# Performance work log

Hardware: AMD Instinct MI355X
Metric: run time of the kernel (lower is better)

Reference implementation:

```python
import jax, jax.numpy as jnp
import numpy as np

LEN_HIS = 20   # q_len_his: sliding-window history length
DIM_C = 4      # dim_c
H = 64         # GRU hidden = final_mlp_hidden_width
D = 36         # global_graph_width(32) + goal(2) + action(2)
N = 32768      # total timesteps across many episodes


def setup_inputs() -> dict:
    key = jax.random.key(0)
    ks = jax.random.split(key, 8)
    emb = jax.random.normal(ks[0], (N, D), jnp.float32)
    dones = (jax.random.uniform(ks[1], (N, 1)) < 0.02).astype(jnp.int32)
    s = lambda k, shape, fan: jax.random.normal(k, shape, jnp.float32) / np.sqrt(fan).astype(np.float32)
    return {
        "embeddings": emb,
        "W_ih": s(ks[2], (3 * H, D), D),
        "W_hh": s(ks[3], (3 * H, H), H),
        "b_ih": jnp.zeros((3 * H,), jnp.float32),
        "b_hh": jnp.zeros((3 * H,), jnp.float32),
        "W1": s(ks[4], (H, H), H),
        "b1": jnp.zeros((H,), jnp.float32),
        "W2": s(ks[5], (DIM_C, H), H),
        "b2": jnp.zeros((DIM_C,), jnp.float32),
        "dones": dones,
    }


def _his_calculate_c(embeddings, W_ih, W_hh, b_ih, b_hh, W1, b1, W2, b2, dones):
    """Batched/padded version of the ragged sliding-window GRU+MLP loop.

    For each timestep t, the torch code runs the GRU over
    embeddings[max(episode_start, t-L+1) : t+1] from a zero hidden state,
    then applies FinalPredMLP to the final hidden state.
    """
    n = embeddings.shape[0]
    done = dones[:, 0] != 0
    idx = jnp.arange(n)
    # episode_start[t] = (index of most recent done strictly before t) + 1, else 0
    prev_done = jnp.concatenate([jnp.zeros((1,), bool), done[:-1]])
    ep_start = jax.lax.cummax(jnp.where(prev_done, idx, 0))
    win_start = jnp.maximum(ep_start, idx - LEN_HIS + 1)            # [N]

    # padded windows: position l holds embeddings[t - (L-1) + l]
    gidx = idx[:, None] - (LEN_HIS - 1) + jnp.arange(LEN_HIS)[None, :]  # [N, L]
    valid = gidx >= win_start[:, None]                                   # [N, L]
    X = embeddings[jnp.clip(gidx, 0, n - 1)] * valid[..., None]          # [N, L, D]

    def cell(h, inp):
        x, v = inp                      # x: [N, D], v: [N]
        gi = x @ W_ih.T + b_ih          # [N, 3H]
        gh = h @ W_hh.T + b_hh          # [N, 3H]
        ir, iz, inn = jnp.split(gi, 3, axis=-1)
        hr, hz, hnn = jnp.split(gh, 3, axis=-1)
        r = jax.nn.sigmoid(ir + hr)
        z = jax.nn.sigmoid(iz + hz)
        ncand = jnp.tanh(inn + r * hnn)
        h_new = (1.0 - z) * ncand + z * h
        return jnp.where(v[:, None], h_new, h), None

    h0 = jnp.zeros((n, H), embeddings.dtype)
    hT, _ = jax.lax.scan(cell, h0, (jnp.swapaxes(X, 0, 1), valid.T))  # [N, H]

    # FinalPredMLP: Linear(H,H) -> ReLU -> Linear(H, dim_c)
    hid = jax.nn.relu(hT @ W1.T + b1)
    return hid @ W2.T + b2              # [N, dim_c]


def reference(embeddings, W_ih, W_hh, b_ih, b_hh, W1, b1, W2, b2, dones):
    return _his_calculate_c(embeddings, W_ih, W_hh, b_ih, b_hh, W1, b1, W2, b2, dones)
```

## Files before the change

### kernel.cpp

```cpp
#include <hip/hip_runtime.h>

#define NT 32768
#define DI 36
#define HH 64
#define G3 192
#define LH 20
#define SGS 196

#define NLOG2E -1.4426950408889634f
#define TLOG2E 2.8853900817779268f

#define UNION_OFF  27440
#define SFIRST_OFF 41264
#define SMEM_BYTES 41328

typedef __attribute__((ext_vector_type(8))) short bf16x8;
typedef __attribute__((ext_vector_type(4))) float f32x4;
typedef __attribute__((ext_vector_type(4))) int int4v;
union frag_cast { int4v i4; bf16x8 h8; };

__device__ __forceinline__ unsigned f2u(float f) { union { float f; unsigned u; } x; x.f = f; return x.u; }
__device__ __forceinline__ float u2f(unsigned u) { union { float f; unsigned u; } x; x.u = u; return x.f; }
__device__ __forceinline__ unsigned short f2bf_rne(float f) {
    union { float f; unsigned u; } x; x.f = f;
    unsigned r = x.u + 0x7FFFu + ((x.u >> 16) & 1u);
    return (unsigned short)(r >> 16);
}

__global__ __launch_bounds__(64) void prep_kernel(
    const float* __restrict__ W_ih, const float* __restrict__ W_hh,
    int4v* __restrict__ wfrag)
{
    const int b = (int)blockIdx.x;
    const int set = b / 24, fb = b % 24;
    const int mt = fb >> 1, kt = fb & 1;
    const int l = (int)threadIdx.x;
    const int m = mt * 16 + (l & 15);
    const int g = mt >> 2;
    const float sc = (g < 2) ? NLOG2E : TLOG2E;
    const int k0 = kt * 32 + (l >> 4) * 8;
    unsigned short e[8];
#pragma unroll
    for (int jj = 0; jj < 8; ++jj) {
        const int k = k0 + jj;
        if (set == 2) {
            e[jj] = f2bf_rne(W_hh[(size_t)m * HH + k] * sc);
        } else {
            const float v = (k < DI) ? W_ih[(size_t)m * DI + k] * sc : 0.f;
            const unsigned u = f2u(v);
            if (set == 0) e[jj] = (unsigned short)(u >> 16);
            else          e[jj] = (unsigned short)(f2u(v - u2f(u & 0xFFFF0000u)) >> 16);
        }
    }
    int4v p;
    p.x = e[0] | ((unsigned)e[1] << 16); p.y = e[2] | ((unsigned)e[3] << 16);
    p.z = e[4] | ((unsigned)e[5] << 16); p.w = e[6] | ((unsigned)e[7] << 16);
    wfrag[b * 64 + l] = p;
}

__global__ __launch_bounds__(256, 3) void gru_kernel(
    const float* __restrict__ emb, const int4v* __restrict__ wfrag,
    const float* __restrict__ b_ih, const float* __restrict__ b_hh,
    const float* __restrict__ W1, const float* __restrict__ b1,
    const float* __restrict__ W2, const float* __restrict__ b2,
    const int* __restrict__ dones, float* __restrict__ out)
{
    __shared__ __align__(16) char SMEM[SMEM_BYTES];
    float* const Sg = (float*)SMEM;
    unsigned short* const EmbH = (unsigned short*)(SMEM + UNION_OFF);
    unsigned short* const EmbL = EmbH + 48 * 72;
    unsigned short* const HbB  = (unsigned short*)(SMEM + UNION_OFF);
    int* const sfirst = (int*)(SMEM + SFIRST_OFF);

    const int tid = threadIdx.x;
    const int lane = tid & 63;
    const int W = tid >> 6;
    const int li = lane & 15;
    const int q = lane >> 4;
    const int blk = ((int)blockIdx.x & 7) * 256 + ((int)blockIdx.x >> 3);
    const int T0 = blk * 16;

    {
        int4v* z = (int4v*)EmbH;
        for (int i = tid; i < (48 * 72 * 2 * 2) / 16; i += 256) z[i] = int4v{0,0,0,0};
    }
    if (tid < 16) {
        const int tt = T0 + tid;
        int lo = tt - (LH - 1); if (lo < 0) lo = 0;
        int ws = lo;
        for (int j = lo; j < tt; ++j)
            ws = (dones[j] != 0) ? (j + 1) : ws;
        sfirst[tid] = ws - (tt - (LH - 1));
    }
    __syncthreads();
    for (int i = tid; i < 35 * DI; i += 256) {
        const int r = i / DI, c = i % DI;
        int tt = T0 - (LH - 1) + r; tt = tt < 0 ? 0 : tt;
        const float v = emb[(size_t)tt * DI + c];
        const unsigned u = f2u(v);
        EmbH[r * 72 + c] = (unsigned short)(u >> 16);
        EmbL[r * 72 + c] = (unsigned short)(f2u(v - u2f(u & 0xFFFF0000u)) >> 16);
    }

    bf16x8 aih[3][2], ail[3][2], whh[3][2];
#pragma unroll
    for (int g = 0; g < 3; ++g)
#pragma unroll
        for (int kt = 0; kt < 2; ++kt) {
            const int fb = (4 * g + W) * 2 + kt;
            frag_cast a, b, c;
            a.i4 = wfrag[(0 * 24 + fb) * 64 + lane];
            b.i4 = wfrag[(1 * 24 + fb) * 64 + lane];
            c.i4 = wfrag[(2 * 24 + fb) * 64 + lane];
            aih[g][kt] = a.h8; ail[g][kt] = b.h8; whh[g][kt] = c.h8;
        }

    const int joff = 16 * W + 4 * q;
    f32x4 biasI[3];
#pragma unroll
    for (int g = 0; g < 3; ++g) {
        const float sc = (g < 2) ? NLOG2E : TLOG2E;
        const f32x4 bi = *(const f32x4*)&b_ih[64 * g + joff];
        if (g < 2) {
            const f32x4 bh = *(const f32x4*)&b_hh[64 * g + joff];
#pragma unroll
            for (int rr = 0; rr < 4; ++rr) biasI[g][rr] = (bi[rr] + bh[rr]) * sc;
        } else {
#pragma unroll
            for (int rr = 0; rr < 4; ++rr) biasI[g][rr] = bi[rr] * sc;
        }
    }
    f32x4 bnv;
    {
        const f32x4 b = *(const f32x4*)&b_hh[128 + joff];
#pragma unroll
        for (int rr = 0; rr < 4; ++rr) bnv[rr] = b[rr] * TLOG2E;
    }
    __syncthreads();

#pragma unroll
    for (int nt = 0; nt < 3; ++nt) {
        bf16x8 ebh[2], ebl[2];
#pragma unroll
        for (int kt = 0; kt < 2; ++kt) {
            const int idx = (16 * nt + li) * 72 + 32 * kt + 8 * q;
            ebh[kt] = *(const bf16x8*)&EmbH[idx];
            ebl[kt] = *(const bf16x8*)&EmbL[idx];
        }
#pragma unroll
        for (int g = 0; g < 3; ++g) {
            f32x4 a = biasI[g];
            a = __builtin_amdgcn_mfma_f32_16x16x32_bf16(aih[g][0], ebh[0], a, 0, 0, 0);
            a = __builtin_amdgcn_mfma_f32_16x16x32_bf16(aih[g][1], ebh[1], a, 0, 0, 0);
            a = __builtin_amdgcn_mfma_f32_16x16x32_bf16(ail[g][0], ebh[0], a, 0, 0, 0);
            a = __builtin_amdgcn_mfma_f32_16x16x32_bf16(ail[g][1], ebh[1], a, 0, 0, 0);
            a = __builtin_amdgcn_mfma_f32_16x16x32_bf16(aih[g][0], ebl[0], a, 0, 0, 0);
            a = __builtin_amdgcn_mfma_f32_16x16x32_bf16(aih[g][1], ebl[1], a, 0, 0, 0);
            const int row = 16 * nt + li;
            if (row < 35)
                *(f32x4*)&Sg[row * SGS + 64 * g + joff] = a;
        }
    }
    __syncthreads();
    const int sfr = sfirst[li];

    float h[4] = {0.f, 0.f, 0.f, 0.f};
    f32x4 accR, accZ, accN, ginv;
    f32x4 gvR, gvZ, gvN;

    {
        const float* gp = Sg + li * SGS;
        accR = *(const f32x4*)(gp + joff);
        accZ = *(const f32x4*)(gp + 64 + joff);
        ginv = *(const f32x4*)(gp + 128 + joff);
        accN = bnv;
        const bool valid = (0 >= sfr);
#pragma unroll
        for (int rr = 0; rr < 4; ++rr) {
            const float r  = __builtin_amdgcn_rcpf(1.f + __builtin_amdgcn_exp2f(accR[rr]));
            const float z  = __builtin_amdgcn_rcpf(1.f + __builtin_amdgcn_exp2f(accZ[rr]));
            const float nc = 1.f - 2.f * __builtin_amdgcn_rcpf(1.f + __builtin_amdgcn_exp2f(ginv[rr] + r * accN[rr]));
            h[rr] = valid ? fmaf(z, 0.f - nc, nc) : 0.f;
        }
        const unsigned u0 = f2u(h[0]), u1 = f2u(h[1]);
        const unsigned u2 = f2u(h[2]), u3 = f2u(h[3]);
        uint2 ph, pl;
        ph.x = __builtin_amdgcn_perm(u1, u0, 0x07060302u);
        ph.y = __builtin_amdgcn_perm(u3, u2, 0x07060302u);
        const unsigned l0 = f2u(h[0] - u2f(u0 & 0xFFFF0000u));
        const unsigned l1 = f2u(h[1] - u2f(u1 & 0xFFFF0000u));
        const unsigned l2 = f2u(h[2] - u2f(u2 & 0xFFFF0000u));
        const unsigned l3 = f2u(h[3] - u2f(u3 & 0xFFFF0000u));
        pl.x = __builtin_amdgcn_perm(l1, l0, 0x07060302u);
        pl.y = __builtin_amdgcn_perm(l3, l2, 0x07060302u);
        *(uint2*)&HbB[1 * 2304 + 0 * 1152 + li * 72 + joff] = ph;
        *(uint2*)&HbB[1 * 2304 + 1 * 1152 + li * 72 + joff] = pl;
        const float* gq = Sg + (li + 1) * SGS;
        gvR = *(const f32x4*)(gq + joff);
        gvZ = *(const f32x4*)(gq + 64 + joff);
        gvN = *(const f32x4*)(gq + 128 + joff);
    }
    __syncthreads();

#pragma unroll 2
    for (int s = 1; s < LH; ++s) {
        const int rb = s & 1;
        const bf16x8 bh0 = *(const bf16x8*)&HbB[rb * 2304 + li * 72 + 8 * q];
        const bf16x8 bh1 = *(const bf16x8*)&HbB[rb * 2304 + li * 72 + 32 + 8 * q];
        const bf16x8 bl0 = *(const bf16x8*)&HbB[rb * 2304 + 1152 + li * 72 + 8 * q];
        const bf16x8 bl1 = *(const bf16x8*)&HbB[rb * 2304 + 1152 + li * 72 + 32 + 8 * q];

        accR = gvR; accZ = gvZ; ginv = gvN; accN = bnv;
        {
            int r = li + s + 1; r = r > 34 ? 34 : r;
            const float* gq = Sg + r * SGS;
            gvR = *(const f32x4*)(gq + joff);
            gvZ = *(const f32x4*)(gq + 64 + joff);
            gvN = *(const f32x4*)(gq + 128 + joff);
        }
#pragma unroll
        for (int g = 0; g < 3; ++g) {
            f32x4 a = (g == 0) ? accR : (g == 1) ? accZ : accN;
            a = __builtin_amdgcn_mfma_f32_16x16x32_bf16(whh[g][0], bh0, a, 0, 0, 0);
            a = __builtin_amdgcn_mfma_f32_16x16x32_bf16(whh[g][1], bh1, a, 0, 0, 0);
            a = __builtin_amdgcn_mfma_f32_16x16x32_bf16(whh[g][0], bl0, a, 0, 0, 0);
            a = __builtin_amdgcn_mfma_f32_16x16x32_bf16(whh[g][1], bl1, a, 0, 0, 0);
            if (g == 0) accR = a; else if (g == 1) accZ = a; else accN = a;
        }
        const bool valid = (s >= sfr);
#pragma unroll
        for (int rr = 0; rr < 4; ++rr) {
            const float r  = __builtin_amdgcn_rcpf(1.f + __builtin_amdgcn_exp2f(accR[rr]));
            const float z  = __builtin_amdgcn_rcpf(1.f + __builtin_amdgcn_exp2f(accZ[rr]));
            const float nc = 1.f - 2.f * __builtin_amdgcn_rcpf(1.f + __builtin_amdgcn_exp2f(ginv[rr] + r * accN[rr]));
            const float hn = fmaf(z, h[rr] - nc, nc);
            h[rr] = valid ? hn : h[rr];
        }
        {
            const unsigned u0 = f2u(h[0]), u1 = f2u(h[1]);
            const unsigned u2 = f2u(h[2]), u3 = f2u(h[3]);
            uint2 ph, pl;
            ph.x = __builtin_amdgcn_perm(u1, u0, 0x07060302u);
            ph.y = __builtin_amdgcn_perm(u3, u2, 0x07060302u);
            const unsigned l0 = f2u(h[0] - u2f(u0 & 0xFFFF0000u));
            const unsigned l1 = f2u(h[1] - u2f(u1 & 0xFFFF0000u));
            const unsigned l2 = f2u(h[2] - u2f(u2 & 0xFFFF0000u));
            const unsigned l3 = f2u(h[3] - u2f(u3 & 0xFFFF0000u));
            pl.x = __builtin_amdgcn_perm(l1, l0, 0x07060302u);
            pl.y = __builtin_amdgcn_perm(l3, l2, 0x07060302u);
            *(uint2*)&HbB[(1 - rb) * 2304 + li * 72 + joff] = ph;
            *(uint2*)&HbB[(1 - rb) * 2304 + 1152 + li * 72 + joff] = pl;
        }
        __syncthreads();
    }

    float* const Hf  = Sg;
    float* const Hid = Sg + 16 * 68;
    {
        float4 st; st.x = h[0]; st.y = h[1]; st.z = h[2]; st.w = h[3];
        *(float4*)&Hf[li * 68 + joff] = st;
    }
    __syncthreads();
    {
        float hid[4] = {0.f, 0.f, 0.f, 0.f};
        for (int k4 = 0; k4 < 16; ++k4) {
            const float4 wv = *(const float4*)&W1[lane * HH + 4 * k4];
#pragma unroll
            for (int tt = 0; tt < 4; ++tt) {
                const float4 hv = *(const float4*)&Hf[(4 * W + tt) * 68 + 4 * k4];
                hid[tt] += hv.x * wv.x + hv.y * wv.y + hv.z * wv.z + hv.w * wv.w;
            }
        }
        const float bb = b1[lane];
#pragma unroll
        for (int tt = 0; tt < 4; ++tt)
            Hid[(4 * W + tt) * 68 + lane] = fmaxf(hid[tt] + bb, 0.f);
    }
    __syncthreads();
    if (tid < 64) {
        const int tt = tid >> 2, c = tid & 3;
        float o2 = b2[c];
        for (int m4 = 0; m4 < 16; ++m4) {
            const float4 hv = *(const float4*)&Hid[tt * 68 + 4 * m4];
            const float4 wv = *(const float4*)&W2[c * HH + 4 * m4];
            o2 += hv.x * wv.x + hv.y * wv.y + hv.z * wv.z + hv.w * wv.w;
        }
        out[(size_t)(T0 + tt) * 4 + c] = o2;
    }
}

extern "C" void kernel_launch(void* const* d_in, const int* in_sizes, int n_in,
                              void* d_out, int out_size, void* d_ws, size_t ws_size,
                              hipStream_t stream) {
    const float* emb  = (const float*)d_in[0];
    const float* W_ih = (const float*)d_in[1];
    const float* W_hh = (const float*)d_in[2];
    const float* b_ih = (const float*)d_in[3];
    const float* b_hh = (const float*)d_in[4];
    const float* W1   = (const float*)d_in[5];
    const float* b1   = (const float*)d_in[6];
    const float* W2   = (const float*)d_in[7];
    const float* b2   = (const float*)d_in[8];
    const int*   dn   = (const int*)d_in[9];

    int4v* wfrag = (int4v*)d_ws;
    float* o = (float*)d_out;

    prep_kernel<<<72, 64, 0, stream>>>(W_ih, W_hh, wfrag);
    gru_kernel<<<NT / 16, 256, 0, stream>>>(emb, wfrag, b_ih, b_hh,
                                            W1, b1, W2, b2, dn, o);
}
```

Before: 133.5 us.

## Drop low-part hidden-state MFMAs, run first MLP layer on MFMA, raise occupancy

The recurrent h@W_hh product now uses only the bf16 high part of the hidden state, which halves the per-step MFMA count and LDS traffic and shrinks the double buffer. The first MLP layer moves from scalar FMA loops to split-bf16 MFMAs, with W1 fragments prepared by extra blocks in the prep kernel. The embedding tile stride is reduced from 72 to 64 and launch bounds go from 3 to 4 blocks per CU, with shared memory trimmed to fit. The cost is lower precision in the recurrence, plus possible LDS bank conflicts from the new stride.

```diff
diff --git a/kernel.cpp b/kernel.cpp
--- a/kernel.cpp
+++ b/kernel.cpp
@@ -11,8 +11,8 @@
 #define TLOG2E 2.8853900817779268f
 
 #define UNION_OFF  27440
-#define SFIRST_OFF 41264
-#define SMEM_BYTES 41328
+#define SFIRST_OFF 39728
+#define SMEM_BYTES 39792
 
 typedef __attribute__((ext_vector_type(8))) short bf16x8;
 typedef __attribute__((ext_vector_type(4))) float f32x4;
@@ -29,27 +29,42 @@
 
 __global__ __launch_bounds__(64) void prep_kernel(
     const float* __restrict__ W_ih, const float* __restrict__ W_hh,
-    int4v* __restrict__ wfrag)
+    const float* __restrict__ W1, int4v* __restrict__ wfrag)
 {
     const int b = (int)blockIdx.x;
-    const int set = b / 24, fb = b % 24;
-    const int mt = fb >> 1, kt = fb & 1;
     const int l = (int)threadIdx.x;
-    const int m = mt * 16 + (l & 15);
-    const int g = mt >> 2;
-    const float sc = (g < 2) ? NLOG2E : TLOG2E;
-    const int k0 = kt * 32 + (l >> 4) * 8;
     unsigned short e[8];
-#pragma unroll
-    for (int jj = 0; jj < 8; ++jj) {
-        const int k = k0 + jj;
-        if (set == 2) {
-            e[jj] = f2bf_rne(W_hh[(size_t)m * HH + k] * sc);
-        } else {
-            const float v = (k < DI) ? W_ih[(size_t)m * DI + k] * sc : 0.f;
+    if (b < 72) {
+        const int set = b / 24, fb = b % 24;
+        const int mt = fb >> 1, kt = fb & 1;
+        const int m = mt * 16 + (l & 15);
+        const float sc = ((mt >> 2) < 2) ? NLOG2E : TLOG2E;
+        const int k0 = kt * 32 + (l >> 4) * 8;
+#pragma unroll
+        for (int jj = 0; jj < 8; ++jj) {
+            const int k = k0 + jj;
+            if (set == 2) {
+                e[jj] = f2bf_rne(W_hh[(size_t)m * HH + k] * sc);
+            } else {
+                const float v = (k < DI) ? W_ih[(size_t)m * DI + k] * sc : 0.f;
+                const unsigned u = f2u(v);
+                if (set == 0) e[jj] = (unsigned short)(u >> 16);
+                else          e[jj] = (unsigned short)(f2u(v - u2f(u & 0xFFFF0000u)) >> 16);
+            }
+        }
+    } else {
+        const int bb = b - 72;
+        const bool is_lo = bb >= 8;
+        const int f = bb & 7;
+        const int mt = f >> 1, kt = f & 1;
+        const int m = mt * 16 + (l & 15);
+        const int k0 = kt * 32 + (l >> 4) * 8;
+#pragma unroll
+        for (int jj = 0; jj < 8; ++jj) {
+            const float v = W1[(size_t)m * HH + k0 + jj];
             const unsigned u = f2u(v);
-            if (set == 0) e[jj] = (unsigned short)(u >> 16);
-            else          e[jj] = (unsigned short)(f2u(v - u2f(u & 0xFFFF0000u)) >> 16);
+            if (!is_lo) e[jj] = (unsigned short)(u >> 16);
+            else        e[jj] = (unsigned short)(f2u(v - u2f(u & 0xFFFF0000u)) >> 16);
         }
     }
     int4v p;
@@ -58,18 +73,20 @@
     wfrag[b * 64 + l] = p;
 }
 
-__global__ __launch_bounds__(256, 3) void gru_kernel(
+__global__ __launch_bounds__(256, 4) void gru_kernel(
     const float* __restrict__ emb, const int4v* __restrict__ wfrag,
     const float* __restrict__ b_ih, const float* __restrict__ b_hh,
-    const float* __restrict__ W1, const float* __restrict__ b1,
-    const float* __restrict__ W2, const float* __restrict__ b2,
-    const int* __restrict__ dones, float* __restrict__ out)
+    const float* __restrict__ b1, const float* __restrict__ W2,
+    const float* __restrict__ b2, const int* __restrict__ dones,
+    float* __restrict__ out)
 {
     __shared__ __align__(16) char SMEM[SMEM_BYTES];
     float* const Sg = (float*)SMEM;
     unsigned short* const EmbH = (unsigned short*)(SMEM + UNION_OFF);
-    unsigned short* const EmbL = EmbH + 48 * 72;
+    unsigned short* const EmbL = EmbH + 48 * 64;
     unsigned short* const HbB  = (unsigned short*)(SMEM + UNION_OFF);
+    unsigned short* const HfH  = (unsigned short*)(SMEM + UNION_OFF);
+    unsigned short* const HfL  = HfH + 1152;
     int* const sfirst = (int*)(SMEM + SFIRST_OFF);
 
     const int tid = threadIdx.x;
@@ -82,7 +99,7 @@
 
     {
         int4v* z = (int4v*)EmbH;
-        for (int i = tid; i < (48 * 72 * 2 * 2) / 16; i += 256) z[i] = int4v{0,0,0,0};
+        for (int i = tid; i < 768; i += 256) z[i] = int4v{0, 0, 0, 0};
     }
     if (tid < 16) {
         const int tt = T0 + tid;
@@ -98,8 +115,8 @@
         int tt = T0 - (LH - 1) + r; tt = tt < 0 ? 0 : tt;
         const float v = emb[(size_t)tt * DI + c];
         const unsigned u = f2u(v);
-        EmbH[r * 72 + c] = (unsigned short)(u >> 16);
-        EmbL[r * 72 + c] = (unsigned short)(f2u(v - u2f(u & 0xFFFF0000u)) >> 16);
+        EmbH[r * 64 + c] = (unsigned short)(u >> 16);
+        EmbL[r * 64 + c] = (unsigned short)(f2u(v - u2f(u & 0xFFFF0000u)) >> 16);
     }
 
     bf16x8 aih[3][2], ail[3][2], whh[3][2];
@@ -143,7 +160,7 @@
         bf16x8 ebh[2], ebl[2];
 #pragma unroll
         for (int kt = 0; kt < 2; ++kt) {
-            const int idx = (16 * nt + li) * 72 + 32 * kt + 8 * q;
+            const int idx = (16 * nt + li) * 64 + 32 * kt + 8 * q;
             ebh[kt] = *(const bf16x8*)&EmbH[idx];
             ebl[kt] = *(const bf16x8*)&EmbL[idx];
         }
@@ -182,6 +199,57 @@
             const float nc = 1.f - 2.f * __builtin_amdgcn_rcpf(1.f + __builtin_amdgcn_exp2f(ginv[rr] + r * accN[rr]));
             h[rr] = valid ? fmaf(z, 0.f - nc, nc) : 0.f;
         }
+        uint2 ph;
+        ph.x = __builtin_amdgcn_perm(f2u(h[1]), f2u(h[0]), 0x07060302u);
+        ph.y = __builtin_amdgcn_perm(f2u(h[3]), f2u(h[2]), 0x07060302u);
+        *(uint2*)&HbB[1152 + li * 72 + joff] = ph;
+        const float* gq = Sg + (li + 1) * SGS;
+        gvR = *(const f32x4*)(gq + joff);
+        gvZ = *(const f32x4*)(gq + 64 + joff);
+        gvN = *(const f32x4*)(gq + 128 + joff);
+    }
+    __syncthreads();
+
+#pragma unroll 2
+    for (int s = 1; s < LH; ++s) {
+        const int rb = s & 1;
+        const bf16x8 bh0 = *(const bf16x8*)&HbB[rb * 1152 + li * 72 + 8 * q];
+        const bf16x8 bh1 = *(const bf16x8*)&HbB[rb * 1152 + li * 72 + 32 + 8 * q];
+
+        accR = gvR; accZ = gvZ; ginv = gvN; accN = bnv;
+        {
+            int r = li + s + 1; r = r > 34 ? 34 : r;
+            const float* gq = Sg + r * SGS;
+            gvR = *(const f32x4*)(gq + joff);
+            gvZ = *(const f32x4*)(gq + 64 + joff);
+            gvN = *(const f32x4*)(gq + 128 + joff);
+        }
+#pragma unroll
+        for (int g = 0; g < 3; ++g) {
+            f32x4 a = (g == 0) ? accR : (g == 1) ? accZ : accN;
+            a = __builtin_amdgcn_mfma_f32_16x16x32_bf16(whh[g][0], bh0, a, 0, 0, 0);
+            a = __builtin_amdgcn_mfma_f32_16x16x32_bf16(whh[g][1], bh1, a, 0, 0, 0);
+            if (g == 0) accR = a; else if (g == 1) accZ = a; else accN = a;
+        }
+        const bool valid = (s >= sfr);
+#pragma unroll
+        for (int rr = 0; rr < 4; ++rr) {
+            const float r  = __builtin_amdgcn_rcpf(1.f + __builtin_amdgcn_exp2f(accR[rr]));
+            const float z  = __builtin_amdgcn_rcpf(1.f + __builtin_amdgcn_exp2f(accZ[rr]));
+            const float nc = 1.f - 2.f * __builtin_amdgcn_rcpf(1.f + __builtin_amdgcn_exp2f(ginv[rr] + r * accN[rr]));
+            const float hn = fmaf(z, h[rr] - nc, nc);
+            h[rr] = valid ? hn : h[rr];
+        }
+        if (s != LH - 1) {
+            uint2 ph;
+            ph.x = __builtin_amdgcn_perm(f2u(h[1]), f2u(h[0]), 0x07060302u);
+            ph.y = __builtin_amdgcn_perm(f2u(h[3]), f2u(h[2]), 0x07060302u);
+            *(uint2*)&HbB[(1 - rb) * 1152 + li * 72 + joff] = ph;
+        }
+        __syncthreads();
+    }
+
+    {
         const unsigned u0 = f2u(h[0]), u1 = f2u(h[1]);
         const unsigned u2 = f2u(h[2]), u3 = f2u(h[3]);
         uint2 ph, pl;
@@ -193,95 +261,42 @@
         const unsigned l3 = f2u(h[3] - u2f(u3 & 0xFFFF0000u));
         pl.x = __builtin_amdgcn_perm(l1, l0, 0x07060302u);
         pl.y = __builtin_amdgcn_perm(l3, l2, 0x07060302u);
-        *(uint2*)&HbB[1 * 2304 + 0 * 1152 + li * 72 + joff] = ph;
-        *(uint2*)&HbB[1 * 2304 + 1 * 1152 + li * 72 + joff] = pl;
-        const float* gq = Sg + (li + 1) * SGS;
-        gvR = *(const f32x4*)(gq + joff);
-        gvZ = *(const f32x4*)(gq + 64 + joff);
-        gvN = *(const f32x4*)(gq + 128 + joff);
-    }
-    __syncthreads();
-
-#pragma unroll 2
-    for (int s = 1; s < LH; ++s) {
-        const int rb = s & 1;
-        const bf16x8 bh0 = *(const bf16x8*)&HbB[rb * 2304 + li * 72 + 8 * q];
-        const bf16x8 bh1 = *(const bf16x8*)&HbB[rb * 2304 + li * 72 + 32 + 8 * q];
-        const bf16x8 bl0 = *(const bf16x8*)&HbB[rb * 2304 + 1152 + li * 72 + 8 * q];
-        const bf16x8 bl1 = *(const bf16x8*)&HbB[rb * 2304 + 1152 + li * 72 + 32 + 8 * q];
-
-        accR = gvR; accZ = gvZ; ginv = gvN; accN = bnv;
-        {
-            int r = li + s + 1; r = r > 34 ? 34 : r;
-            const float* gq = Sg + r * SGS;
-            gvR = *(const f32x4*)(gq + joff);
-            gvZ = *(const f32x4*)(gq + 64 + joff);
-            gvN = *(const f32x4*)(gq + 128 + joff);
-        }
-#pragma unroll
-        for (int g = 0; g < 3; ++g) {
-            f32x4 a = (g == 0) ? accR : (g == 1) ? accZ : accN;
-            a = __builtin_amdgcn_mfma_f32_16x16x32_bf16(whh[g][0], bh0, a, 0, 0, 0);
-            a = __builtin_amdgcn_mfma_f32_16x16x32_bf16(whh[g][1], bh1, a, 0, 0, 0);
-            a = __builtin_amdgcn_mfma_f32_16x16x32_bf16(whh[g][0], bl0, a, 0, 0, 0);
-            a = __builtin_amdgcn_mfma_f32_16x16x32_bf16(whh[g][1], bl1, a, 0, 0, 0);
-            if (g == 0) accR = a; else if (g == 1) accZ = a; else accN = a;
-        }
-        const bool valid = (s >= sfr);
-#pragma unroll
-        for (int rr = 0; rr < 4; ++rr) {
-            const float r  = __builtin_amdgcn_rcpf(1.f + __builtin_amdgcn_exp2f(accR[rr]));
-            const float z  = __builtin_amdgcn_rcpf(1.f + __builtin_amdgcn_exp2f(accZ[rr]));
-            const float nc = 1.f - 2.f * __builtin_amdgcn_rcpf(1.f + __builtin_amdgcn_exp2f(ginv[rr] + r * accN[rr]));
-            const float hn = fmaf(z, h[rr] - nc, nc);
-            h[rr] = valid ? hn : h[rr];
-        }
-        {
-            const unsigned u0 = f2u(h[0]), u1 = f2u(h[1]);
-            const unsigned u2 = f2u(h[2]), u3 = f2u(h[3]);
-            uint2 ph, pl;
-            ph.x = __builtin_amdgcn_perm(u1, u0, 0x07060302u);
-            ph.y = __builtin_amdgcn_perm(u3, u2, 0x07060302u);
-            const unsigned l0 = f2u(h[0] - u2f(u0 & 0xFFFF0000u));
-            const unsigned l1 = f2u(h[1] - u2f(u1 & 0xFFFF0000u));
-            const unsigned l2 = f2u(h[2] - u2f(u2 & 0xFFFF0000u));
-            const unsigned l3 = f2u(h[3] - u2f(u3 & 0xFFFF0000u));
-            pl.x = __builtin_amdgcn_perm(l1, l0, 0x07060302u);
-            pl.y = __builtin_amdgcn_perm(l3, l2, 0x07060302u);
-            *(uint2*)&HbB[(1 - rb) * 2304 + li * 72 + joff] = ph;
-            *(uint2*)&HbB[(1 - rb) * 2304 + 1152 + li * 72 + joff] = pl;
-        }
+        *(uint2*)&HfH[li * 72 + joff] = ph;
+        *(uint2*)&HfL[li * 72 + joff] = pl;
+    }
+    __syncthreads();
+    {
+        bf16x8 w1h[2], w1l[2];
+#pragma unroll
+        for (int kt = 0; kt < 2; ++kt) {
+            frag_cast a, b;
+            a.i4 = wfrag[(72 + W * 2 + kt) * 64 + lane];
+            b.i4 = wfrag[(80 + W * 2 + kt) * 64 + lane];
+            w1h[kt] = a.h8; w1l[kt] = b.h8;
+        }
+        const bf16x8 bh0 = *(const bf16x8*)&HfH[li * 72 + 8 * q];
+        const bf16x8 bh1 = *(const bf16x8*)&HfH[li * 72 + 32 + 8 * q];
+        const bf16x8 bl0 = *(const bf16x8*)&HfL[li * 72 + 8 * q];
+        const bf16x8 bl1 = *(const bf16x8*)&HfL[li * 72 + 32 + 8 * q];
+        f32x4 a = *(const f32x4*)&b1[joff];
+        a = __builtin_amdgcn_mfma_f32_16x16x32_bf16(w1h[0], bh0, a, 0, 0, 0);
+        a = __builtin_amdgcn_mfma_f32_16x16x32_bf16(w1h[1], bh1, a, 0, 0, 0);
+        a = __builtin_amdgcn_mfma_f32_16x16x32_bf16(w1l[0], bh0, a, 0, 0, 0);
+        a = __builtin_amdgcn_mfma_f32_16x16x32_bf16(w1l[1], bh1, a, 0, 0, 0);
+        a = __builtin_amdgcn_mfma_f32_16x16x32_bf16(w1h[0], bl0, a, 0, 0, 0);
+        a = __builtin_amdgcn_mfma_f32_16x16x32_bf16(w1h[1], bl1, a, 0, 0, 0);
         __syncthreads();
-    }
-
-    float* const Hf  = Sg;
-    float* const Hid = Sg + 16 * 68;
-    {
-        float4 st; st.x = h[0]; st.y = h[1]; st.z = h[2]; st.w = h[3];
-        *(float4*)&Hf[li * 68 + joff] = st;
-    }
-    __syncthreads();
-    {
-        float hid[4] = {0.f, 0.f, 0.f, 0.f};
-        for (int k4 = 0; k4 < 16; ++k4) {
-            const float4 wv = *(const float4*)&W1[lane * HH + 4 * k4];
-#pragma unroll
-            for (int tt = 0; tt < 4; ++tt) {
-                const float4 hv = *(const float4*)&Hf[(4 * W + tt) * 68 + 4 * k4];
-                hid[tt] += hv.x * wv.x + hv.y * wv.y + hv.z * wv.z + hv.w * wv.w;
-            }
-        }
-        const float bb = b1[lane];
-#pragma unroll
-        for (int tt = 0; tt < 4; ++tt)
-            Hid[(4 * W + tt) * 68 + lane] = fmaxf(hid[tt] + bb, 0.f);
+        float4 st;
+        st.x = fmaxf(a[0], 0.f); st.y = fmaxf(a[1], 0.f);
+        st.z = fmaxf(a[2], 0.f); st.w = fmaxf(a[3], 0.f);
+        *(float4*)&Sg[li * 68 + joff] = st;
     }
     __syncthreads();
     if (tid < 64) {
         const int tt = tid >> 2, c = tid & 3;
         float o2 = b2[c];
         for (int m4 = 0; m4 < 16; ++m4) {
-            const float4 hv = *(const float4*)&Hid[tt * 68 + 4 * m4];
+            const float4 hv = *(const float4*)&Sg[tt * 68 + 4 * m4];
             const float4 wv = *(const float4*)&W2[c * HH + 4 * m4];
             o2 += hv.x * wv.x + hv.y * wv.y + hv.z * wv.z + hv.w * wv.w;
         }
@@ -306,7 +321,7 @@
     int4v* wfrag = (int4v*)d_ws;
     float* o = (float*)d_out;
 
-    prep_kernel<<<72, 64, 0, stream>>>(W_ih, W_hh, wfrag);
+    prep_kernel<<<88, 64, 0, stream>>>(W_ih, W_hh, W1, wfrag);
     gru_kernel<<<NT / 16, 256, 0, stream>>>(emb, wfrag, b_ih, b_hh,
-                                            W1, b1, W2, b2, dn, o);
+                                            b1, W2, b2, dn, o);
 }
```

Result: faster. 114.8 us (-14.0%).
